# Performance work log

Hardware: AMD Instinct MI355X
Metric: run time of the kernel (lower is better)

## Reference

```python
import jax, jax.numpy as jnp
import numpy as np

B, N, FEAT, H, E, L = 4096, 64, 32, 128, 4, 3  # batch, node_num, node feat, hidden_dim, edge_dim, hidden_num


def setup_inputs() -> dict:
    key = jax.random.key(0)
    ks = jax.random.split(key, 12)
    s = 0.05
    x = jax.random.normal(ks[0], (B, N, FEAT), dtype=jnp.float32)
    adj = jax.random.uniform(ks[1], (B, E, N, N), dtype=jnp.float32)
    # per-node input/output embeddings (stacked over node index)
    in_w = jax.random.normal(ks[2], (N, FEAT, H), dtype=jnp.float32) * s
    in_b = jax.random.normal(ks[3], (N, H), dtype=jnp.float32) * s
    out_w = jax.random.normal(ks[4], (N, H, FEAT), dtype=jnp.float32) * s
    out_b = jax.random.normal(ks[5], (N, FEAT), dtype=jnp.float32) * s
    # relational GC weights per layer: (L, E, H, H) and bias (L, E, 1, H)
    gc_w = jax.random.normal(ks[6], (L, E, H, H), dtype=jnp.float32) * s
    gc_b = jax.random.normal(ks[7], (L, E, 1, H), dtype=jnp.float32) * s
    # GRU params, gate order [r, z, n] like torch
    w_ih = jax.random.normal(ks[8], (3 * H, H), dtype=jnp.float32) * s
    w_hh = jax.random.normal(ks[9], (3 * H, H), dtype=jnp.float32) * s
    b_ih = jax.random.normal(ks[10], (3 * H,), dtype=jnp.float32) * s
    b_hh = jax.random.normal(ks[11], (3 * H,), dtype=jnp.float32) * s
    return {"x": x, "adj": adj, "in_w": in_w, "in_b": in_b, "out_w": out_w,
            "out_b": out_b, "gc_w": gc_w, "gc_b": gc_b, "w_ih": w_ih,
            "w_hh": w_hh, "b_ih": b_ih, "b_hh": b_hh}


def _gru_step(xf, h, w_ih, w_hh, b_ih, b_hh):
    # xf, h: (B*N, H); single-timestep torch GRU cell
    gi = xf @ w_ih.T + b_ih
    gh = h @ w_hh.T + b_hh
    i_r, i_z, i_n = jnp.split(gi, 3, axis=-1)
    h_r, h_z, h_n = jnp.split(gh, 3, axis=-1)
    r = jax.nn.sigmoid(i_r + h_r)
    z = jax.nn.sigmoid(i_z + h_z)
    n = jnp.tanh(i_n + r * h_n)
    return (1.0 - z) * n + z * h


def reference(x, adj, in_w, in_b, out_w, out_b, gc_w, gc_b, w_ih, w_hh, b_ih, b_hh):
    # per-node input embedding: (B, N, FEAT) -> (B, N, H)
    h = jnp.einsum('bnd,ndh->bnh', x, in_w) + in_b
    hidden = h.reshape(-1, H)  # initial GRU hidden = embedded input
    cur = h
    for i in range(L):
        # relational GCN: per-edge-type projection + adjacency matmul + bias + relu + mean over edge types
        support = jnp.einsum('bid,edh->beih', cur, gc_w[i])
        out = jnp.einsum('beij,bejh->beih', adj, support) + gc_b[i]
        out = jax.nn.relu(out)
        agg = jnp.mean(out, axis=1)  # (B, N, H)
        hidden = _gru_step(agg.reshape(-1, H), hidden, w_ih, w_hh, b_ih, b_hh)
        cur = hidden.reshape(B, N, H)
    # per-node output embedding, zero-padded back to hidden width
    feats = jnp.einsum('bnh,nhd->bnd', cur, out_w) + out_b  # (B, N, FEAT)
    return jnp.pad(feats, ((0, 0), (0, 0), (0, H - FEAT)))
```

## Files before the change

### kernel.cpp

```cpp
#include <hip/hip_runtime.h>
#include <cstdint>

#define NBATCH 4096
#define NNODE  64
#define FEAT   32
#define H      128
#define NE     4
#define NL     3

typedef __attribute__((ext_vector_type(8))) short short8;
typedef __attribute__((ext_vector_type(4))) short short4v;
typedef __attribute__((ext_vector_type(4))) float f32x4;
typedef __attribute__((ext_vector_type(2))) float f32x2;
typedef unsigned long long u64;
typedef unsigned short ushort;

#define IMG_GC_ELEMS   (128 * 64)
#define IMG_GRU_ELEMS  (48 * 128)
#define IMG_GC_BYTES   (24 * IMG_GC_ELEMS * 2)
#define IMG_GRU_BYTES  (16 * IMG_GRU_ELEMS * 2)
#define WS_W_BYTES     (IMG_GC_BYTES + IMG_GRU_BYTES)
#define WIMG_SHORTS    (WS_W_BYTES / 2)
#define ADJ_IMG_ELEMS  4096
#define WS_FULL ((size_t)WS_W_BYTES + (size_t)NBATCH * NE * ADJ_IMG_ELEMS * 2)

__device__ __forceinline__ ushort f2b(float f) {
  union { float f; unsigned u; } v; v.f = f;
  unsigned u = v.u + 0x7FFFu + ((v.u >> 16) & 1u);
  return (ushort)(u >> 16);
}
__device__ __forceinline__ float b2f(ushort s) {
  union { unsigned u; float f; } v; v.u = ((unsigned)s) << 16;
  return v.f;
}
__device__ __forceinline__ unsigned cvtpk(float lo, float hi) {
  unsigned r;
  asm volatile("v_cvt_pk_bf16_f32 %0, %1, %2" : "=v"(r) : "v"(lo), "v"(hi));
  return r;
}
__device__ __forceinline__ u64 pk4(float a, float b, float c, float d) {
  return (u64)cvtpk(a, b) | ((u64)cvtpk(c, d) << 32);
}
__device__ __forceinline__ float sigm(float v) { return 1.0f / (1.0f + __expf(-v)); }
__device__ __forceinline__ float tanh_(float v) {
  v = fminf(fmaxf(v, -15.f), 15.f);
  float e = __expf(-2.f * v);
  return (1.f - e) / (1.f + e);
}
__device__ __forceinline__ int gidx128(int r, int g) { return r * 128 + ((g ^ (r & 7)) << 3); }
__device__ __forceinline__ int idx128(int r, int k) { return gidx128(r, k >> 3) + (k & 7); }
__device__ __forceinline__ int gidx64(int r, int g) { return r * 64 + (((g ^ (r & 7)) & 7) << 3); }

__device__ __forceinline__ short8 pack8f(const float* v) {
  union { unsigned u[4]; short8 s; } r;
  r.u[0] = cvtpk(v[0], v[1]); r.u[1] = cvtpk(v[2], v[3]);
  r.u[2] = cvtpk(v[4], v[5]); r.u[3] = cvtpk(v[6], v[7]);
  return r.s;
}

__device__ __forceinline__ void gll16(const void* g, void* l) {
  __builtin_amdgcn_global_load_lds(
      (const __attribute__((address_space(1))) unsigned int*)g,
      (__attribute__((address_space(3))) unsigned int*)l, 16, 0, 0);
}

#define STAGE(dst, src, NIT)                                             \
  do {                                                                   \
    _Pragma("unroll")                                                    \
    for (int it_ = 0; it_ < (NIT); ++it_) {                              \
      int off_ = (it_ * 4 + w) * 1024;                                   \
      gll16((const char*)(src) + off_ + lane * 16, (char*)(dst) + off_); \
    }                                                                    \
  } while (0)

#define BAR() do { asm volatile("s_waitcnt lgkmcnt(0)" ::: "memory"); \
                   __builtin_amdgcn_s_barrier(); } while (0)
#define VMW(N) do { asm volatile("s_waitcnt vmcnt(" #N ")" ::: "memory"); \
                    __builtin_amdgcn_sched_barrier(0); } while (0)
#define SB0() __builtin_amdgcn_sched_barrier(0)

__global__ __launch_bounds__(256, 2) void k_prep(
    const float* __restrict__ gc_w, const float* __restrict__ w_ih,
    const float* __restrict__ w_hh, ushort* __restrict__ ws)
{
  const int t = threadIdx.x;
  if (blockIdx.x < 24) {
    const int blk = blockIdx.x;
    const int kh = blk & 1, e = (blk >> 1) & 3, l = blk >> 3;
    const float* We = gc_w + (size_t)(l * NE + e) * H * H;
    ushort* dst = ws + (size_t)blk * IMG_GC_ELEMS;
    #pragma unroll
    for (int it = 0; it < 4; ++it) {
      int idx = t + it * 256;
      int r = idx >> 3, g = idx & 7;
      float v[8];
      #pragma unroll
      for (int j = 0; j < 8; ++j) v[j] = We[(kh * 64 + g * 8 + j) * H + r];
      *(short8*)&dst[gidx64(r, g)] = pack8f(v);
    }
  } else {
    const int blk = blockIdx.x - 24;
    const int c = blk & 7, m = blk >> 3;
    const float* Mat = m ? w_hh : w_ih;
    ushort* dst = ws + WIMG_SHORTS - IMG_GRU_BYTES / 2 + (size_t)blk * IMG_GRU_ELEMS;
    #pragma unroll
    for (int it = 0; it < 3; ++it) {
      int idx = t + it * 256;
      int rr = idx >> 4, g = idx & 15;
      int mrow = (rr >> 4) * H + 16 * c + (rr & 15);
      float v[8];
      #pragma unroll
      for (int j = 0; j < 8; ++j) v[j] = Mat[mrow * H + g * 8 + j];
      *(short8*)&dst[gidx128(rr, g)] = pack8f(v);
    }
  }
}

template <bool ADJIMG>
__global__ __launch_bounds__(256, 2) void k_inemb(
    const float* __restrict__ x, const float* __restrict__ in_w,
    const float* __restrict__ in_b, const float* __restrict__ adj,
    ushort* __restrict__ ws, float* __restrict__ out)
{
  __shared__ float s_wt[FEAT * H];
  __shared__ float s_x[64 * FEAT];
  const int t = threadIdx.x;
  const int n = blockIdx.x >> 6, bt = blockIdx.x & 63, b0 = bt * 64;
  const float* wsrc = in_w + (size_t)n * FEAT * H;
  #pragma unroll
  for (int it = 0; it < 4; ++it) {
    int i4 = t + it * 256;
    *(f32x4*)&s_wt[i4 * 4] = *(const f32x4*)&wsrc[i4 * 4];
  }
  {
    int r = t >> 2, q = t & 3;
    const float* xs = x + ((size_t)(b0 + r) * NNODE + n) * FEAT;
    *(f32x4*)&s_x[r * 32 + q * 8]     = *(const f32x4*)&xs[q * 8];
    *(f32x4*)&s_x[r * 32 + q * 8 + 4] = *(const f32x4*)&xs[q * 8 + 4];
  }
  __syncthreads();
  const int h2 = t & 63, rp = t >> 6;
  const float bi0 = in_b[n * H + 2 * h2], bi1 = in_b[n * H + 2 * h2 + 1];
  #pragma unroll 1
  for (int m = 0; m < 16; ++m) {
    int r = rp + 4 * m;
    float a0 = bi0, a1 = bi1;
    #pragma unroll
    for (int d = 0; d < 32; ++d) {
      float xv = s_x[r * 32 + d];
      f32x2 wv = *(const f32x2*)&s_wt[d * H + 2 * h2];
      a0 += xv * wv.x; a1 += xv * wv.y;
    }
    unsigned p = cvtpk(a0, a1);
    ushort* tail = (ushort*)(out + ((size_t)(b0 + r) * NNODE + n) * H + 64);
    *(unsigned*)(tail + 2 * h2) = p;
  }
  if (ADJIMG) {
    const float* ab = adj + (size_t)blockIdx.x * NE * NNODE * NNODE;
    ushort* dst = ws + WIMG_SHORTS + (size_t)blockIdx.x * NE * ADJ_IMG_ELEMS;
    #pragma unroll 1
    for (int q = 0; q < 8; ++q) {
      int gi = t + q * 256;
      int e = gi >> 9, idx = gi & 511, r = idx >> 3, g = idx & 7;
      const float* src = ab + e * 4096 + r * 64 + g * 8;
      float v[8];
      #pragma unroll
      for (int j = 0; j < 8; ++j) v[j] = src[j];
      *(short8*)&dst[e * ADJ_IMG_ELEMS + gidx64(r, g)] = pack8f(v);
    }
  }
}

template <bool ADJIMG>
__global__ __launch_bounds__(256, 2) void k_main(
    const float* __restrict__ adj,
    const float* __restrict__ gc_b,
    const float* __restrict__ b_ih, const float* __restrict__ b_hh,
    const ushort* __restrict__ wimg,
    float* __restrict__ out)
{
  __shared__ ushort s_u[128 * 64];
  __shared__ ushort s_stage[24576];
  __shared__ float s_bias[1280];

  ushort* w0    = s_stage;
  ushort* w1    = s_stage + 8192;
  ushort* sadj  = s_stage + 16384;
  ushort* gru0  = s_stage;
  ushort* gru1  = s_stage + 12288;

  const int t = threadIdx.x;
  const int b = blockIdx.x;
  const int w = t >> 6, lane = t & 63, lr = lane & 15, lq = lane >> 4;
  const int wm = w & 1, wn = w >> 1;
  float* outb = out + (size_t)b * NNODE * H;
  const ushort* img_gru = wimg + WIMG_SHORTS - IMG_GRU_BYTES / 2;
  const ushort* aimg = wimg + WIMG_SHORTS + (size_t)b * NE * ADJ_IMG_ELEMS;

  STAGE(w0, wimg, 4);
  short8 cur[2][4];
  #pragma unroll
  for (int rt = 0; rt < 2; ++rt)
    #pragma unroll
    for (int ks = 0; ks < 4; ++ks) {
      int node = 32 * wm + 16 * rt + lr;
      cur[rt][ks] = *(const short8*)((const ushort*)(outb + (size_t)node * H + 64) + 32 * ks + 8 * lq);
    }
  #pragma unroll
  for (int it = 0; it < 3; ++it) {
    int idx = t + it * 256;
    s_bias[512 + idx] = (idx < 384) ? b_ih[idx] : b_hh[idx - 384];
  }
  __syncthreads();

  #pragma unroll 1
  for (int layer = 0; layer < NL; ++layer) {
    f32x4 agg[2][4];
    #pragma unroll
    for (int mt = 0; mt < 2; ++mt)
      #pragma unroll
      for (int nt = 0; nt < 4; ++nt) agg[mt][nt] = f32x4{0.f, 0.f, 0.f, 0.f};

    #pragma unroll 1
    for (int e = 0; e < NE; ++e) {
      const ushort* img_e = wimg + (size_t)((layer * NE + e) * 2) * IMG_GC_ELEMS;

      if (e == 0) {
        s_bias[t]       = gc_b[layer * 512 + t];
        s_bias[t + 256] = gc_b[layer * 512 + t + 256];
      }
      STAGE(w1, img_e + IMG_GC_ELEMS, 4);
      SB0();
      if (ADJIMG) {
        STAGE(sadj, aimg + (size_t)e * ADJ_IMG_ELEMS, 2);
        SB0();
      } else {
        const float* adj_e = adj + (((size_t)b * NE + e) * NNODE * NNODE);
        #pragma unroll
        for (int it = 0; it < 2; ++it) {
          int idx = t + it * 256;
          int i = idx >> 3, g = idx & 7;
          const float* src = adj_e + i * 64 + g * 8;
          float v[8];
          #pragma unroll
          for (int j = 0; j < 8; ++j) v[j] = src[j];
          *(short8*)&sadj[gidx64(i, g)] = pack8f(v);
        }
      }
      f32x4 Sacc[2][4];
      #pragma unroll
      for (int mt = 0; mt < 2; ++mt)
        #pragma unroll
        for (int nt = 0; nt < 4; ++nt) Sacc[mt][nt] = f32x4{0.f, 0.f, 0.f, 0.f};
      if (ADJIMG) VMW(6);
      __builtin_amdgcn_s_setprio(1);
      #pragma unroll
      for (int ks = 0; ks < 2; ++ks) {
        #pragma unroll
        for (int nt = 0; nt < 4; ++nt) {
          short8 bb = *(const short8*)&w0[gidx64(64 * wn + 16 * nt + lr, ks * 4 + lq)];
          #pragma unroll
          for (int mt = 0; mt < 2; ++mt)
            Sacc[mt][nt] = __builtin_amdgcn_mfma_f32_16x16x32_bf16(cur[mt][ks], bb, Sacc[mt][nt], 0, 0, 0);
        }
      }
      __builtin_amdgcn_s_setprio(0);
      if (ADJIMG) { VMW(2); BAR(); } else __syncthreads();

      if (e < 3) { STAGE(w0, img_e + 2 * IMG_GC_ELEMS, 4); }
      else       { STAGE(gru0, img_gru, 3); }
      SB0();
      __builtin_amdgcn_s_setprio(1);
      #pragma unroll
      for (int ks = 0; ks < 2; ++ks) {
        #pragma unroll
        for (int nt = 0; nt < 4; ++nt) {
          short8 bb = *(const short8*)&w1[gidx64(64 * wn + 16 * nt + lr, ks * 4 + lq)];
          #pragma unroll
          for (int mt = 0; mt < 2; ++mt)
            Sacc[mt][nt] = __builtin_amdgcn_mfma_f32_16x16x32_bf16(cur[mt][2 + ks], bb, Sacc[mt][nt], 0, 0, 0);
        }
      }
      __builtin_amdgcn_s_setprio(0);
      #pragma unroll
      for (int mt = 0; mt < 2; ++mt) {
        int j0 = 32 * wm + 16 * mt + 4 * lq;
        #pragma unroll
        for (int nt = 0; nt < 4; ++nt) {
          int h = 64 * wn + 16 * nt + lr;
          *(u64*)&s_u[gidx64(h, j0 >> 3) + (j0 & 7)] =
              pk4(Sacc[mt][nt][0], Sacc[mt][nt][1], Sacc[mt][nt][2], Sacc[mt][nt][3]);
        }
      }
      if (ADJIMG) { if (e < 3) { VMW(4); } else { VMW(3); } BAR(); } else __syncthreads();

      if (e == 3) { STAGE(gru0 + 6144, img_gru + IMG_GRU_ELEMS, 3); SB0(); }
      {
        f32x4 Oacc[2][4];
        #pragma unroll
        for (int mt = 0; mt < 2; ++mt)
          #pragma unroll
          for (int nt = 0; nt < 4; ++nt) Oacc[mt][nt] = f32x4{0.f, 0.f, 0.f, 0.f};
        __builtin_amdgcn_s_setprio(1);
        #pragma unroll
        for (int ks = 0; ks < 2; ++ks) {
          short8 a[2];
          #pragma unroll
          for (int mt = 0; mt < 2; ++mt)
            a[mt] = *(const short8*)&sadj[gidx64(32 * wm + 16 * mt + lr, ks * 4 + lq)];
          #pragma unroll
          for (int nt = 0; nt < 4; ++nt) {
            short8 bb = *(const short8*)&s_u[gidx64(64 * wn + 16 * nt + lr, ks * 4 + lq)];
            #pragma unroll
            for (int mt = 0; mt < 2; ++mt)
              Oacc[mt][nt] = __builtin_amdgcn_mfma_f32_16x16x32_bf16(a[mt], bb, Oacc[mt][nt], 0, 0, 0);
          }
        }
        __builtin_amdgcn_s_setprio(0);
        #pragma unroll
        for (int mt = 0; mt < 2; ++mt)
          #pragma unroll
          for (int nt = 0; nt < 4; ++nt) {
            float bias = s_bias[e * 128 + 64 * wn + 16 * nt + lr];
            #pragma unroll
            for (int r = 0; r < 4; ++r)
              agg[mt][nt][r] += 0.25f * fmaxf(Oacc[mt][nt][r] + bias, 0.f);
          }
      }
      if (ADJIMG) { BAR(); } else __syncthreads();
    }

    #pragma unroll
    for (int mt = 0; mt < 2; ++mt)
      #pragma unroll
      for (int nt = 0; nt < 4; ++nt) {
        int h = 64 * wn + 16 * nt + lr;
        #pragma unroll
        for (int r = 0; r < 4; ++r)
          s_u[idx128(32 * wm + 16 * mt + 4 * lq + r, h)] = f2b(agg[mt][nt][r]);
      }
    __syncthreads();

    #pragma unroll 1
    for (int p = 0; p < 4; ++p) {
      const int cc = 2 * p + wn;
      const ushort* ihb = gru0 + wn * 6144;
      const ushort* hhb = gru1 + wn * 6144;
      STAGE(gru1, img_gru + (size_t)(8 + 2 * p) * IMG_GRU_ELEMS, 3);
      STAGE(gru1 + 6144, img_gru + (size_t)(8 + 2 * p + 1) * IMG_GRU_ELEMS, 3);
      SB0();
      short4v holdv[2];
      #pragma unroll
      for (int nst = 0; nst < 2; ++nst) {
        int node = 16 * (2 * wm + nst) + lr;
        holdv[nst] = *(const short4v*)((const ushort*)(outb + (size_t)node * H + 64) + 16 * cc + 4 * lq);
      }
      f32x4 gi[3][2];
      #pragma unroll
      for (int tg = 0; tg < 3; ++tg)
        #pragma unroll
        for (int nst = 0; nst < 2; ++nst) gi[tg][nst] = f32x4{0.f, 0.f, 0.f, 0.f};
      __builtin_amdgcn_s_setprio(1);
      #pragma unroll
      for (int ks = 0; ks < 4; ++ks) {
        short8 bb[2];
        #pragma unroll
        for (int nst = 0; nst < 2; ++nst)
          bb[nst] = *(const short8*)&s_u[gidx128(16 * (2 * wm + nst) + lr, ks * 4 + lq)];
        #pragma unroll
        for (int tg = 0; tg < 3; ++tg) {
          short8 a = *(const short8*)&ihb[gidx128(16 * tg + lr, ks * 4 + lq)];
          #pragma unroll
          for (int nst = 0; nst < 2; ++nst)
            gi[tg][nst] = __builtin_amdgcn_mfma_f32_16x16x32_bf16(a, bb[nst], gi[tg][nst], 0, 0, 0);
        }
      }
      __builtin_amdgcn_s_setprio(0);
      __syncthreads();

      if (p < 3) {
        STAGE(gru0, img_gru + (size_t)(2 * (p + 1)) * IMG_GRU_ELEMS, 3);
        STAGE(gru0 + 6144, img_gru + (size_t)(2 * (p + 1) + 1) * IMG_GRU_ELEMS, 3);
      } else if (layer < 2) {
        STAGE(w0, wimg + (size_t)((layer + 1) * NE * 2) * IMG_GC_ELEMS, 4);
      }
      SB0();
      f32x4 gh[3][2];
      #pragma unroll
      for (int tg = 0; tg < 3; ++tg)
        #pragma unroll
        for (int nst = 0; nst < 2; ++nst) gh[tg][nst] = f32x4{0.f, 0.f, 0.f, 0.f};
      __builtin_amdgcn_s_setprio(1);
      #pragma unroll
      for (int ks = 0; ks < 4; ++ks) {
        #pragma unroll
        for (int tg = 0; tg < 3; ++tg) {
          short8 a = *(const short8*)&hhb[gidx128(16 * tg + lr, ks * 4 + lq)];
          #pragma unroll
          for (int nst = 0; nst < 2; ++nst)
            gh[tg][nst] = __builtin_amdgcn_mfma_f32_16x16x32_bf16(a, cur[nst][ks], gh[tg][nst], 0, 0, 0);
        }
      }
      __builtin_amdgcn_s_setprio(0);
      #pragma unroll
      for (int nst = 0; nst < 2; ++nst) {
        int node = 16 * (2 * wm + nst) + lr;
        float hf[4];
        #pragma unroll
        for (int r = 0; r < 4; ++r) {
          int mH = 16 * cc + 4 * lq + r;
          float rg = sigm(gi[0][nst][r] + s_bias[512 + mH] + gh[0][nst][r] + s_bias[896 + mH]);
          float zg = sigm(gi[1][nst][r] + s_bias[640 + mH] + gh[1][nst][r] + s_bias[1024 + mH]);
          float ng = tanh_(gi[2][nst][r] + s_bias[768 + mH] + rg * (gh[2][nst][r] + s_bias[1152 + mH]));
          float hold = b2f((ushort)holdv[nst][r]);
          hf[r] = (1.f - zg) * ng + zg * hold;
        }
        *(u64*)((ushort*)(outb + (size_t)node * H + 64) + 16 * cc + 4 * lq) =
            pk4(hf[0], hf[1], hf[2], hf[3]);
      }
      __syncthreads();
    }

    if (layer < 2) {
      #pragma unroll
      for (int rt = 0; rt < 2; ++rt)
        #pragma unroll
        for (int ks = 0; ks < 4; ++ks) {
          int node = 32 * wm + 16 * rt + lr;
          cur[rt][ks] = *(const short8*)((const ushort*)(outb + (size_t)node * H + 64) + 32 * ks + 8 * lq);
        }
    }
  }
}

__global__ __launch_bounds__(256, 2) void k_outemb(
    const float* __restrict__ out_w, const float* __restrict__ out_b,
    float* __restrict__ out)
{
  __shared__ float s_wt[H * FEAT];
  __shared__ float s_c[64 * 132];
  const int t = threadIdx.x;
  const int n = blockIdx.x >> 6, bt = blockIdx.x & 63, b0 = bt * 64;
  const float* wsrc = out_w + (size_t)n * H * FEAT;
  #pragma unroll
  for (int it = 0; it < 4; ++it) {
    int i4 = t + it * 256;
    *(f32x4*)&s_wt[i4 * 4] = *(const f32x4*)&wsrc[i4 * 4];
  }
  #pragma unroll
  for (int it = 0; it < 4; ++it) {
    int idx = t + it * 256;
    int r = idx >> 4, g = idx & 15;
    const ushort* tail = (const ushort*)(out + ((size_t)(b0 + r) * NNODE + n) * H + 64);
    short8 v = *(const short8*)(tail + g * 8);
    #pragma unroll
    for (int j = 0; j < 8; ++j) s_c[r * 132 + g * 8 + j] = b2f((ushort)v[j]);
  }
  __syncthreads();
  const int d = t & 31, rq = t >> 5;
  const float bias = out_b[n * FEAT + d];
  float accs[8];
  #pragma unroll
  for (int m = 0; m < 8; ++m) {
    int r = rq + 8 * m;
    float a = bias;
    #pragma unroll 8
    for (int k = 0; k < H; ++k) a += s_c[r * 132 + k] * s_wt[k * FEAT + d];
    accs[m] = a;
  }
  #pragma unroll
  for (int m = 0; m < 8; ++m) {
    int r = rq + 8 * m;
    out[((size_t)(b0 + r) * NNODE + n) * H + d] = accs[m];
  }
  #pragma unroll
  for (int q = 0; q < 6; ++q) {
    int idx = t + q * 256;
    int r = idx / 24, c4 = idx - r * 24;
    *(f32x4*)&out[((size_t)(b0 + r) * NNODE + n) * H + FEAT + c4 * 4] =
        f32x4{0.f, 0.f, 0.f, 0.f};
  }
}

extern "C" void kernel_launch(void* const* d_in, const int* in_sizes, int n_in,
                              void* d_out, int out_size, void* d_ws, size_t ws_size,
                              hipStream_t stream) {
  const float* x     = (const float*)d_in[0];
  const float* adj   = (const float*)d_in[1];
  const float* in_w  = (const float*)d_in[2];
  const float* in_b  = (const float*)d_in[3];
  const float* out_w = (const float*)d_in[4];
  const float* out_b = (const float*)d_in[5];
  const float* gc_w  = (const float*)d_in[6];
  const float* gc_b  = (const float*)d_in[7];
  const float* w_ih  = (const float*)d_in[8];
  const float* w_hh  = (const float*)d_in[9];
  const float* b_ih  = (const float*)d_in[10];
  const float* b_hh  = (const float*)d_in[11];
  (void)in_sizes; (void)n_in; (void)out_size;
  ushort* wimg = (ushort*)d_ws;
  const bool full = ws_size >= WS_FULL;
  hipLaunchKernelGGL(k_prep, dim3(40), dim3(256), 0, stream, gc_w, w_ih, w_hh, wimg);
  if (full) {
    hipLaunchKernelGGL(k_inemb<true>, dim3(NBATCH), dim3(256), 0, stream,
                       x, in_w, in_b, adj, wimg, (float*)d_out);
    hipLaunchKernelGGL(k_main<true>, dim3(NBATCH), dim3(256), 0, stream,
                       adj, gc_b, b_ih, b_hh, wimg, (float*)d_out);
  } else {
    hipLaunchKernelGGL(k_inemb<false>, dim3(NBATCH), dim3(256), 0, stream,
                       x, in_w, in_b, adj, wimg, (float*)d_out);
    hipLaunchKernelGGL(k_main<false>, dim3(NBATCH), dim3(256), 0, stream,
                       adj, gc_b, b_ih, b_hh, wimg, (float*)d_out);
  }
  hipLaunchKernelGGL(k_outemb, dim3(NBATCH), dim3(256), 0, stream, out_w, out_b, (float*)d_out);
}
```

Measured before the change: 763.9 us.

## Run main GNN kernel with 8 waves and triple-buffered weight staging

Doubles the main kernel's block to 512 threads so each wave owns a smaller output tile (half the columns in GCN, one node group in GRU). It reorganises LDS into three rotating weight buffers plus a separate adjacency buffer, so the next edge-type's weight halves can be prefetched earlier. GC biases move into registers and GRU bias indexing is compacted. The aim is more latency hiding and occupancy, at the cost of more waves contending for barriers and higher LDS use per block, which may limit how many blocks fit per CU.

```diff
diff --git a/kernel.cpp b/kernel.cpp
--- a/kernel.cpp
+++ b/kernel.cpp
@@ -64,11 +64,11 @@
       (__attribute__((address_space(3))) unsigned int*)l, 16, 0, 0);
 }
 
-#define STAGE(dst, src, NIT)                                             \
+#define STAGE8(dst, src, NIT)                                            \
   do {                                                                   \
     _Pragma("unroll")                                                    \
     for (int it_ = 0; it_ < (NIT); ++it_) {                              \
-      int off_ = (it_ * 4 + w) * 1024;                                   \
+      int off_ = (it_ * 8 + w) * 1024;                                   \
       gll16((const char*)(src) + off_ + lane * 16, (char*)(dst) + off_); \
     }                                                                    \
   } while (0)
@@ -78,6 +78,8 @@
 #define VMW(N) do { asm volatile("s_waitcnt vmcnt(" #N ")" ::: "memory"); \
                     __builtin_amdgcn_sched_barrier(0); } while (0)
 #define SB0() __builtin_amdgcn_sched_barrier(0)
+
+#define MFMA16(A, B, C) __builtin_amdgcn_mfma_f32_16x16x32_bf16((A), (B), (C), 0, 0, 0)
 
 __global__ __launch_bounds__(256, 2) void k_prep(
     const float* __restrict__ gc_w, const float* __restrict__ w_ih,
@@ -172,113 +174,111 @@
 }
 
 template <bool ADJIMG>
-__global__ __launch_bounds__(256, 2) void k_main(
+__global__ __launch_bounds__(512, 4) void k_main(
     const float* __restrict__ adj,
     const float* __restrict__ gc_b,
     const float* __restrict__ b_ih, const float* __restrict__ b_hh,
     const ushort* __restrict__ wimg,
     float* __restrict__ out)
 {
-  __shared__ ushort s_u[128 * 64];
-  __shared__ ushort s_stage[24576];
-  __shared__ float s_bias[1280];
-
-  ushort* w0    = s_stage;
-  ushort* w1    = s_stage + 8192;
-  ushort* sadj  = s_stage + 16384;
-  ushort* gru0  = s_stage;
-  ushort* gru1  = s_stage + 12288;
+  __shared__ ushort s_stage[28672];
+  __shared__ ushort s_u[8192];
+  __shared__ float  s_bias[768];
+
+  ushort* const R0   = s_stage;
+  ushort* const R1   = s_stage + 8192;
+  ushort* const R2   = s_stage + 16384;
+  ushort* const adjb = s_stage + 24576;
+  ushort* const G0   = s_stage;
+  ushort* const G1   = s_stage + 12288;
 
   const int t = threadIdx.x;
   const int b = blockIdx.x;
   const int w = t >> 6, lane = t & 63, lr = lane & 15, lq = lane >> 4;
-  const int wm = w & 1, wn = w >> 1;
+  const int wm = w & 1, wq = w >> 1;
+  const int cpar = wq & 1, nsub = wq >> 1;
+  const int ng = 2 * wm + nsub;
   float* outb = out + (size_t)b * NNODE * H;
-  const ushort* img_gru = wimg + WIMG_SHORTS - IMG_GRU_BYTES / 2;
+  const ushort* img_gruih = wimg + 196608;
+  const ushort* img_gruhh = wimg + 196608 + 8 * IMG_GRU_ELEMS;
   const ushort* aimg = wimg + WIMG_SHORTS + (size_t)b * NE * ADJ_IMG_ELEMS;
 
-  STAGE(w0, wimg, 4);
-  short8 cur[2][4];
-  #pragma unroll
-  for (int rt = 0; rt < 2; ++rt)
-    #pragma unroll
-    for (int ks = 0; ks < 4; ++ks) {
-      int node = 32 * wm + 16 * rt + lr;
-      cur[rt][ks] = *(const short8*)((const ushort*)(outb + (size_t)node * H + 64) + 32 * ks + 8 * lq);
-    }
-  #pragma unroll
-  for (int it = 0; it < 3; ++it) {
-    int idx = t + it * 256;
-    s_bias[512 + idx] = (idx < 384) ? b_ih[idx] : b_hh[idx - 384];
-  }
+  ushort* const K0s[4] = {R0, R2, R1, R0};
+  ushort* const K1s[4] = {R1, R0, R2, R1};
+
+  STAGE8(R0, wimg, 2);
+  STAGE8(R1, wimg + 8192, 2);
+  short8 curA[4], curB[4], curS[4];
+  #pragma unroll
+  for (int ks = 0; ks < 4; ++ks) {
+    curA[ks] = *(const short8*)((const ushort*)(outb + (size_t)(32 * wm + lr) * H + 64) + 32 * ks + 8 * lq);
+    curB[ks] = *(const short8*)((const ushort*)(outb + (size_t)(32 * wm + 16 + lr) * H + 64) + 32 * ks + 8 * lq);
+    curS[ks] = *(const short8*)((const ushort*)(outb + (size_t)(16 * ng + lr) * H + 64) + 32 * ks + 8 * lq);
+  }
+  float gb[4][2];
+  #pragma unroll
+  for (int e = 0; e < 4; ++e) {
+    gb[e][0] = gc_b[e * 128 + 32 * wq + lr];
+    gb[e][1] = gc_b[e * 128 + 32 * wq + 16 + lr];
+  }
+  s_bias[t] = (t < 384) ? b_ih[t] : b_hh[t - 384];
+  if (t < 256) s_bias[512 + t] = b_hh[t + 128];
   __syncthreads();
 
   #pragma unroll 1
   for (int layer = 0; layer < NL; ++layer) {
-    f32x4 agg[2][4];
-    #pragma unroll
-    for (int mt = 0; mt < 2; ++mt)
-      #pragma unroll
-      for (int nt = 0; nt < 4; ++nt) agg[mt][nt] = f32x4{0.f, 0.f, 0.f, 0.f};
-
-    #pragma unroll 1
-    for (int e = 0; e < NE; ++e) {
-      const ushort* img_e = wimg + (size_t)((layer * NE + e) * 2) * IMG_GC_ELEMS;
-
-      if (e == 0) {
-        s_bias[t]       = gc_b[layer * 512 + t];
-        s_bias[t + 256] = gc_b[layer * 512 + t + 256];
-      }
-      STAGE(w1, img_e + IMG_GC_ELEMS, 4);
-      SB0();
+    f32x4 agg[2][2];
+    #pragma unroll
+    for (int mt = 0; mt < 2; ++mt) {
+      #pragma unroll
+      for (int nt = 0; nt < 2; ++nt) agg[mt][nt] = f32x4{0.f, 0.f, 0.f, 0.f};
+    }
+
+    #pragma unroll
+    for (int e = 0; e < 4; ++e) {
       if (ADJIMG) {
-        STAGE(sadj, aimg + (size_t)e * ADJ_IMG_ELEMS, 2);
+        STAGE8(adjb, aimg + (size_t)e * ADJ_IMG_ELEMS, 1);
         SB0();
       } else {
         const float* adj_e = adj + (((size_t)b * NE + e) * NNODE * NNODE);
-        #pragma unroll
-        for (int it = 0; it < 2; ++it) {
-          int idx = t + it * 256;
-          int i = idx >> 3, g = idx & 7;
-          const float* src = adj_e + i * 64 + g * 8;
-          float v[8];
-          #pragma unroll
-          for (int j = 0; j < 8; ++j) v[j] = src[j];
-          *(short8*)&sadj[gidx64(i, g)] = pack8f(v);
-        }
-      }
-      f32x4 Sacc[2][4];
-      #pragma unroll
-      for (int mt = 0; mt < 2; ++mt)
-        #pragma unroll
-        for (int nt = 0; nt < 4; ++nt) Sacc[mt][nt] = f32x4{0.f, 0.f, 0.f, 0.f};
-      if (ADJIMG) VMW(6);
+        int i = t >> 3, g = t & 7;
+        const float* src = adj_e + i * 64 + g * 8;
+        float v[8];
+        #pragma unroll
+        for (int j = 0; j < 8; ++j) v[j] = src[j];
+        *(short8*)&adjb[gidx64(i, g)] = pack8f(v);
+      }
+      f32x4 Sacc[2][2];
+      #pragma unroll
+      for (int mt = 0; mt < 2; ++mt) {
+        #pragma unroll
+        for (int nt = 0; nt < 2; ++nt) Sacc[mt][nt] = f32x4{0.f, 0.f, 0.f, 0.f};
+      }
       __builtin_amdgcn_s_setprio(1);
       #pragma unroll
       for (int ks = 0; ks < 2; ++ks) {
         #pragma unroll
-        for (int nt = 0; nt < 4; ++nt) {
-          short8 bb = *(const short8*)&w0[gidx64(64 * wn + 16 * nt + lr, ks * 4 + lq)];
-          #pragma unroll
-          for (int mt = 0; mt < 2; ++mt)
-            Sacc[mt][nt] = __builtin_amdgcn_mfma_f32_16x16x32_bf16(cur[mt][ks], bb, Sacc[mt][nt], 0, 0, 0);
+        for (int nt = 0; nt < 2; ++nt) {
+          short8 bb = *(const short8*)&K0s[e][gidx64(32 * wq + 16 * nt + lr, ks * 4 + lq)];
+          Sacc[0][nt] = MFMA16(curA[ks], bb, Sacc[0][nt]);
+          Sacc[1][nt] = MFMA16(curB[ks], bb, Sacc[1][nt]);
         }
       }
       __builtin_amdgcn_s_setprio(0);
-      if (ADJIMG) { VMW(2); BAR(); } else __syncthreads();
-
-      if (e < 3) { STAGE(w0, img_e + 2 * IMG_GC_ELEMS, 4); }
-      else       { STAGE(gru0, img_gru, 3); }
-      SB0();
+      if (ADJIMG) { VMW(1); BAR(); } else __syncthreads();
+
+      if (e < 3) {
+        STAGE8(K0s[e + 1], wimg + (size_t)((layer * 4 + e + 1) * 2) * IMG_GC_ELEMS, 2);
+        SB0();
+      }
       __builtin_amdgcn_s_setprio(1);
       #pragma unroll
       for (int ks = 0; ks < 2; ++ks) {
         #pragma unroll
-        for (int nt = 0; nt < 4; ++nt) {
-          short8 bb = *(const short8*)&w1[gidx64(64 * wn + 16 * nt + lr, ks * 4 + lq)];
-          #pragma unroll
-          for (int mt = 0; mt < 2; ++mt)
-            Sacc[mt][nt] = __builtin_amdgcn_mfma_f32_16x16x32_bf16(cur[mt][2 + ks], bb, Sacc[mt][nt], 0, 0, 0);
+        for (int nt = 0; nt < 2; ++nt) {
+          short8 bb = *(const short8*)&K1s[e][gidx64(32 * wq + 16 * nt + lr, ks * 4 + lq)];
+          Sacc[0][nt] = MFMA16(curA[2 + ks], bb, Sacc[0][nt]);
+          Sacc[1][nt] = MFMA16(curB[2 + ks], bb, Sacc[1][nt]);
         }
       }
       __builtin_amdgcn_s_setprio(0);
@@ -286,149 +286,137 @@
       for (int mt = 0; mt < 2; ++mt) {
         int j0 = 32 * wm + 16 * mt + 4 * lq;
         #pragma unroll
-        for (int nt = 0; nt < 4; ++nt) {
-          int h = 64 * wn + 16 * nt + lr;
+        for (int nt = 0; nt < 2; ++nt) {
+          int h = 32 * wq + 16 * nt + lr;
           *(u64*)&s_u[gidx64(h, j0 >> 3) + (j0 & 7)] =
               pk4(Sacc[mt][nt][0], Sacc[mt][nt][1], Sacc[mt][nt][2], Sacc[mt][nt][3]);
         }
       }
-      if (ADJIMG) { if (e < 3) { VMW(4); } else { VMW(3); } BAR(); } else __syncthreads();
-
-      if (e == 3) { STAGE(gru0 + 6144, img_gru + IMG_GRU_ELEMS, 3); SB0(); }
+      if (ADJIMG) { if (e < 3) { VMW(2); } else { VMW(0); } BAR(); } else __syncthreads();
+
+      if (e < 3) {
+        STAGE8(K1s[e + 1], wimg + (size_t)((layer * 4 + e + 1) * 2 + 1) * IMG_GC_ELEMS, 2);
+        SB0();
+      } else {
+        STAGE8(G0, img_gruih, 3);
+        STAGE8(G1, img_gruhh, 3);
+        SB0();
+      }
       {
-        f32x4 Oacc[2][4];
-        #pragma unroll
-        for (int mt = 0; mt < 2; ++mt)
+        f32x4 Oacc[2][2];
+        #pragma unroll
+        for (int mt = 0; mt < 2; ++mt) {
           #pragma unroll
-          for (int nt = 0; nt < 4; ++nt) Oacc[mt][nt] = f32x4{0.f, 0.f, 0.f, 0.f};
+          for (int nt = 0; nt < 2; ++nt) Oacc[mt][nt] = f32x4{0.f, 0.f, 0.f, 0.f};
+        }
         __builtin_amdgcn_s_setprio(1);
         #pragma unroll
         for (int ks = 0; ks < 2; ++ks) {
-          short8 a[2];
+          short8 a0 = *(const short8*)&adjb[gidx64(32 * wm + lr, ks * 4 + lq)];
+          short8 a1 = *(const short8*)&adjb[gidx64(32 * wm + 16 + lr, ks * 4 + lq)];
           #pragma unroll
-          for (int mt = 0; mt < 2; ++mt)
-            a[mt] = *(const short8*)&sadj[gidx64(32 * wm + 16 * mt + lr, ks * 4 + lq)];
+          for (int nt = 0; nt < 2; ++nt) {
+            short8 bb = *(const short8*)&s_u[gidx64(32 * wq + 16 * nt + lr, ks * 4 + lq)];
+            Oacc[0][nt] = MFMA16(a0, bb, Oacc[0][nt]);
+            Oacc[1][nt] = MFMA16(a1, bb, Oacc[1][nt]);
+          }
+        }
+        __builtin_amdgcn_s_setprio(0);
+        #pragma unroll
+        for (int mt = 0; mt < 2; ++mt) {
           #pragma unroll
-          for (int nt = 0; nt < 4; ++nt) {
-            short8 bb = *(const short8*)&s_u[gidx64(64 * wn + 16 * nt + lr, ks * 4 + lq)];
-            #pragma unroll
-            for (int mt = 0; mt < 2; ++mt)
-              Oacc[mt][nt] = __builtin_amdgcn_mfma_f32_16x16x32_bf16(a[mt], bb, Oacc[mt][nt], 0, 0, 0);
-          }
-        }
-        __builtin_amdgcn_s_setprio(0);
-        #pragma unroll
-        for (int mt = 0; mt < 2; ++mt)
-          #pragma unroll
-          for (int nt = 0; nt < 4; ++nt) {
-            float bias = s_bias[e * 128 + 64 * wn + 16 * nt + lr];
+          for (int nt = 0; nt < 2; ++nt) {
             #pragma unroll
             for (int r = 0; r < 4; ++r)
-              agg[mt][nt][r] += 0.25f * fmaxf(Oacc[mt][nt][r] + bias, 0.f);
+              agg[mt][nt][r] += 0.25f * fmaxf(Oacc[mt][nt][r] + gb[e][nt], 0.f);
           }
-      }
-      if (ADJIMG) { BAR(); } else __syncthreads();
-    }
-
-    #pragma unroll
-    for (int mt = 0; mt < 2; ++mt)
-      #pragma unroll
-      for (int nt = 0; nt < 4; ++nt) {
-        int h = 64 * wn + 16 * nt + lr;
+        }
+      }
+      if (ADJIMG) { if (e < 3) { VMW(2); } BAR(); } else __syncthreads();
+    }
+
+    #pragma unroll
+    for (int mt = 0; mt < 2; ++mt) {
+      #pragma unroll
+      for (int nt = 0; nt < 2; ++nt) {
+        int h = 32 * wq + 16 * nt + lr;
         #pragma unroll
         for (int r = 0; r < 4; ++r)
           s_u[idx128(32 * wm + 16 * mt + 4 * lq + r, h)] = f2b(agg[mt][nt][r]);
       }
+    }
     __syncthreads();
 
     #pragma unroll 1
     for (int p = 0; p < 4; ++p) {
-      const int cc = 2 * p + wn;
-      const ushort* ihb = gru0 + wn * 6144;
-      const ushort* hhb = gru1 + wn * 6144;
-      STAGE(gru1, img_gru + (size_t)(8 + 2 * p) * IMG_GRU_ELEMS, 3);
-      STAGE(gru1 + 6144, img_gru + (size_t)(8 + 2 * p + 1) * IMG_GRU_ELEMS, 3);
+      const int cc = 2 * p + cpar;
+      if (p >= 1) { STAGE8(G1, img_gruhh + (size_t)p * 12288, 3); }
       SB0();
-      short4v holdv[2];
-      #pragma unroll
-      for (int nst = 0; nst < 2; ++nst) {
-        int node = 16 * (2 * wm + nst) + lr;
-        holdv[nst] = *(const short4v*)((const ushort*)(outb + (size_t)node * H + 64) + 16 * cc + 4 * lq);
-      }
-      f32x4 gi[3][2];
-      #pragma unroll
-      for (int tg = 0; tg < 3; ++tg)
-        #pragma unroll
-        for (int nst = 0; nst < 2; ++nst) gi[tg][nst] = f32x4{0.f, 0.f, 0.f, 0.f};
+      short4v holdv = *(const short4v*)((const ushort*)(outb + (size_t)(16 * ng + lr) * H + 64) + 16 * cc + 4 * lq);
+      f32x4 gi[3], gh[3];
+      #pragma unroll
+      for (int tg = 0; tg < 3; ++tg) gi[tg] = f32x4{0.f, 0.f, 0.f, 0.f};
+      const ushort* ihb = G0 + cpar * 6144;
       __builtin_amdgcn_s_setprio(1);
       #pragma unroll
       for (int ks = 0; ks < 4; ++ks) {
-        short8 bb[2];
-        #pragma unroll
-        for (int nst = 0; nst < 2; ++nst)
-          bb[nst] = *(const short8*)&s_u[gidx128(16 * (2 * wm + nst) + lr, ks * 4 + lq)];
+        short8 bb = *(const short8*)&s_u[gidx128(16 * ng + lr, ks * 4 + lq)];
         #pragma unroll
         for (int tg = 0; tg < 3; ++tg) {
           short8 a = *(const short8*)&ihb[gidx128(16 * tg + lr, ks * 4 + lq)];
-          #pragma unroll
-          for (int nst = 0; nst < 2; ++nst)
-            gi[tg][nst] = __builtin_amdgcn_mfma_f32_16x16x32_bf16(a, bb[nst], gi[tg][nst], 0, 0, 0);
+          gi[tg] = MFMA16(a, bb, gi[tg]);
         }
       }
       __builtin_amdgcn_s_setprio(0);
       __syncthreads();
 
-      if (p < 3) {
-        STAGE(gru0, img_gru + (size_t)(2 * (p + 1)) * IMG_GRU_ELEMS, 3);
-        STAGE(gru0 + 6144, img_gru + (size_t)(2 * (p + 1) + 1) * IMG_GRU_ELEMS, 3);
-      } else if (layer < 2) {
-        STAGE(w0, wimg + (size_t)((layer + 1) * NE * 2) * IMG_GC_ELEMS, 4);
-      }
+      if (p < 3)          { STAGE8(G0, img_gruih + (size_t)(p + 1) * 12288, 3); }
+      else if (layer < 2) { STAGE8(R0, wimg + (size_t)((layer + 1) * 8) * IMG_GC_ELEMS, 2); }
       SB0();
-      f32x4 gh[3][2];
-      #pragma unroll
-      for (int tg = 0; tg < 3; ++tg)
-        #pragma unroll
-        for (int nst = 0; nst < 2; ++nst) gh[tg][nst] = f32x4{0.f, 0.f, 0.f, 0.f};
+      #pragma unroll
+      for (int tg = 0; tg < 3; ++tg) gh[tg] = f32x4{0.f, 0.f, 0.f, 0.f};
+      const ushort* hhb = G1 + cpar * 6144;
       __builtin_amdgcn_s_setprio(1);
       #pragma unroll
       for (int ks = 0; ks < 4; ++ks) {
         #pragma unroll
         for (int tg = 0; tg < 3; ++tg) {
           short8 a = *(const short8*)&hhb[gidx128(16 * tg + lr, ks * 4 + lq)];
-          #pragma unroll
-          for (int nst = 0; nst < 2; ++nst)
-            gh[tg][nst] = __builtin_amdgcn_mfma_f32_16x16x32_bf16(a, cur[nst][ks], gh[tg][nst], 0, 0, 0);
+          gh[tg] = MFMA16(a, curS[ks], gh[tg]);
         }
       }
       __builtin_amdgcn_s_setprio(0);
-      #pragma unroll
-      for (int nst = 0; nst < 2; ++nst) {
-        int node = 16 * (2 * wm + nst) + lr;
+      {
         float hf[4];
         #pragma unroll
         for (int r = 0; r < 4; ++r) {
           int mH = 16 * cc + 4 * lq + r;
-          float rg = sigm(gi[0][nst][r] + s_bias[512 + mH] + gh[0][nst][r] + s_bias[896 + mH]);
-          float zg = sigm(gi[1][nst][r] + s_bias[640 + mH] + gh[1][nst][r] + s_bias[1024 + mH]);
-          float ng = tanh_(gi[2][nst][r] + s_bias[768 + mH] + rg * (gh[2][nst][r] + s_bias[1152 + mH]));
-          float hold = b2f((ushort)holdv[nst][r]);
-          hf[r] = (1.f - zg) * ng + zg * hold;
-        }
-        *(u64*)((ushort*)(outb + (size_t)node * H + 64) + 16 * cc + 4 * lq) =
+          float rg = sigm(gi[0][r] + s_bias[mH] + gh[0][r] + s_bias[384 + mH]);
+          float zg = sigm(gi[1][r] + s_bias[128 + mH] + gh[1][r] + s_bias[512 + mH]);
+          float nn = tanh_(gi[2][r] + s_bias[256 + mH] + rg * (gh[2][r] + s_bias[640 + mH]));
+          hf[r] = (1.f - zg) * nn + zg * b2f((ushort)holdv[r]);
+        }
+        *(u64*)((ushort*)(outb + (size_t)(16 * ng + lr) * H + 64) + 16 * cc + 4 * lq) =
             pk4(hf[0], hf[1], hf[2], hf[3]);
       }
       __syncthreads();
     }
 
     if (layer < 2) {
-      #pragma unroll
-      for (int rt = 0; rt < 2; ++rt)
-        #pragma unroll
-        for (int ks = 0; ks < 4; ++ks) {
-          int node = 32 * wm + 16 * rt + lr;
-          cur[rt][ks] = *(const short8*)((const ushort*)(outb + (size_t)node * H + 64) + 32 * ks + 8 * lq);
-        }
+      STAGE8(R1, wimg + (size_t)((layer + 1) * 8 + 1) * IMG_GC_ELEMS, 2);
+      SB0();
+      #pragma unroll
+      for (int ks = 0; ks < 4; ++ks) {
+        curA[ks] = *(const short8*)((const ushort*)(outb + (size_t)(32 * wm + lr) * H + 64) + 32 * ks + 8 * lq);
+        curB[ks] = *(const short8*)((const ushort*)(outb + (size_t)(32 * wm + 16 + lr) * H + 64) + 32 * ks + 8 * lq);
+        curS[ks] = *(const short8*)((const ushort*)(outb + (size_t)(16 * ng + lr) * H + 64) + 32 * ks + 8 * lq);
+      }
+      #pragma unroll
+      for (int e = 0; e < 4; ++e) {
+        gb[e][0] = gc_b[(layer + 1) * 512 + e * 128 + 32 * wq + lr];
+        gb[e][1] = gc_b[(layer + 1) * 512 + e * 128 + 32 * wq + 16 + lr];
+      }
+      __syncthreads();
     }
   }
 }
@@ -504,12 +492,12 @@
   if (full) {
     hipLaunchKernelGGL(k_inemb<true>, dim3(NBATCH), dim3(256), 0, stream,
                        x, in_w, in_b, adj, wimg, (float*)d_out);
-    hipLaunchKernelGGL(k_main<true>, dim3(NBATCH), dim3(256), 0, stream,
+    hipLaunchKernelGGL(k_main<true>, dim3(NBATCH), dim3(512), 0, stream,
                        adj, gc_b, b_ih, b_hh, wimg, (float*)d_out);
   } else {
     hipLaunchKernelGGL(k_inemb<false>, dim3(NBATCH), dim3(256), 0, stream,
                        x, in_w, in_b, adj, wimg, (float*)d_out);
-    hipLaunchKernelGGL(k_main<false>, dim3(NBATCH), dim3(256), 0, stream,
+    hipLaunchKernelGGL(k_main<false>, dim3(NBATCH), dim3(512), 0, stream,
                        adj, gc_b, b_ih, b_hh, wimg, (float*)d_out);
   }
   hipLaunchKernelGGL(k_outemb, dim3(NBATCH), dim3(256), 0, stream, out_w, out_b, (float*)d_out);
```

New measurement: 1.254 ms. 64.2% more time.

## Switch GCN matmuls to 32x32x16 MFMA and restructure weight staging schedule

Applied to the files above, without the earlier changes.

Replaces the 16x16x32 bf16 MFMA tiles in the relational GCN support and adjacency products with 32x32x16 tiles, changing per-wave fragment layouts, LDS read patterns and the bias/relu accumulation mapping. Weight-image staging is rescheduled so both W0 and W1 halves are prefetched earlier (at kernel start and at end of the previous layer), and the per-edge loop is fully unrolled. The aim is fewer MFMA issues and LDS fragment loads per FLOP and better overlap of global-to-LDS copies with compute. The cost is more accumulator registers (f32x16) and subtler vmcnt/barrier sequencing, which could hurt occupancy or correctness.

```diff
diff --git a/kernel.cpp b/kernel.cpp
--- a/kernel.cpp
+++ b/kernel.cpp
@@ -10,6 +10,7 @@
 
 typedef __attribute__((ext_vector_type(8))) short short8;
 typedef __attribute__((ext_vector_type(4))) short short4v;
+typedef __attribute__((ext_vector_type(16))) float f32x16;
 typedef __attribute__((ext_vector_type(4))) float f32x4;
 typedef __attribute__((ext_vector_type(2))) float f32x2;
 typedef unsigned long long u64;
@@ -48,8 +49,13 @@
   return (1.f - e) / (1.f + e);
 }
 __device__ __forceinline__ int gidx128(int r, int g) { return r * 128 + ((g ^ (r & 7)) << 3); }
-__device__ __forceinline__ int idx128(int r, int k) { return gidx128(r, k >> 3) + (k & 7); }
 __device__ __forceinline__ int gidx64(int r, int g) { return r * 64 + (((g ^ (r & 7)) & 7) << 3); }
+__device__ __forceinline__ f32x16 z16() {
+  f32x16 z;
+  #pragma unroll
+  for (int i = 0; i < 16; ++i) z[i] = 0.f;
+  return z;
+}
 
 __device__ __forceinline__ short8 pack8f(const float* v) {
   union { unsigned u[4]; short8 s; } r;
@@ -78,6 +84,9 @@
 #define VMW(N) do { asm volatile("s_waitcnt vmcnt(" #N ")" ::: "memory"); \
                     __builtin_amdgcn_sched_barrier(0); } while (0)
 #define SB0() __builtin_amdgcn_sched_barrier(0)
+
+#define MFMA16(A, B, C) __builtin_amdgcn_mfma_f32_16x16x32_bf16((A), (B), (C), 0, 0, 0)
+#define MFMA32(A, B, C) __builtin_amdgcn_mfma_f32_32x32x16_bf16((A), (B), (C), 0, 0, 0)
 
 __global__ __launch_bounds__(256, 2) void k_prep(
     const float* __restrict__ gc_w, const float* __restrict__ w_ih,
@@ -179,33 +188,30 @@
     const ushort* __restrict__ wimg,
     float* __restrict__ out)
 {
-  __shared__ ushort s_u[128 * 64];
   __shared__ ushort s_stage[24576];
-  __shared__ float s_bias[1280];
-
-  ushort* w0    = s_stage;
-  ushort* w1    = s_stage + 8192;
-  ushort* sadj  = s_stage + 16384;
-  ushort* gru0  = s_stage;
-  ushort* gru1  = s_stage + 12288;
-
-  const int t = threadIdx.x;
-  const int b = blockIdx.x;
-  const int w = t >> 6, lane = t & 63, lr = lane & 15, lq = lane >> 4;
+  __shared__ ushort s_u[8192];
+  __shared__ float  s_bias[1280];
+
+  ushort* const W0   = s_stage;
+  ushort* const W1   = s_stage + 8192;
+  ushort* const adjb = s_stage + 16384;
+  ushort* const G0   = s_stage;
+  ushort* const G1   = s_stage + 12288;
+
+  const int t = threadIdx.x, b = blockIdx.x;
+  const int w = t >> 6, lane = t & 63, l31 = lane & 31, hi = lane >> 5;
+  const int lr = lane & 15, lq = lane >> 4;
   const int wm = w & 1, wn = w >> 1;
   float* outb = out + (size_t)b * NNODE * H;
   const ushort* img_gru = wimg + WIMG_SHORTS - IMG_GRU_BYTES / 2;
   const ushort* aimg = wimg + WIMG_SHORTS + (size_t)b * NE * ADJ_IMG_ELEMS;
 
-  STAGE(w0, wimg, 4);
-  short8 cur[2][4];
-  #pragma unroll
-  for (int rt = 0; rt < 2; ++rt)
-    #pragma unroll
-    for (int ks = 0; ks < 4; ++ks) {
-      int node = 32 * wm + 16 * rt + lr;
-      cur[rt][ks] = *(const short8*)((const ushort*)(outb + (size_t)node * H + 64) + 32 * ks + 8 * lq);
-    }
+  STAGE(W0, wimg, 4);
+  STAGE(W1, wimg + IMG_GC_ELEMS, 4);
+  short8 cur32[8];
+  #pragma unroll
+  for (int ks = 0; ks < 8; ++ks)
+    cur32[ks] = *(const short8*)((const ushort*)(outb + (size_t)(32 * wm + l31) * H + 64) + 16 * ks + 8 * hi);
   #pragma unroll
   for (int it = 0; it < 3; ++it) {
     int idx = t + it * 256;
@@ -215,24 +221,19 @@
 
   #pragma unroll 1
   for (int layer = 0; layer < NL; ++layer) {
-    f32x4 agg[2][4];
-    #pragma unroll
-    for (int mt = 0; mt < 2; ++mt)
-      #pragma unroll
-      for (int nt = 0; nt < 4; ++nt) agg[mt][nt] = f32x4{0.f, 0.f, 0.f, 0.f};
-
-    #pragma unroll 1
-    for (int e = 0; e < NE; ++e) {
+    f32x16 agg[2];
+    agg[0] = z16(); agg[1] = z16();
+
+    #pragma unroll
+    for (int e = 0; e < 4; ++e) {
       const ushort* img_e = wimg + (size_t)((layer * NE + e) * 2) * IMG_GC_ELEMS;
 
       if (e == 0) {
         s_bias[t]       = gc_b[layer * 512 + t];
         s_bias[t + 256] = gc_b[layer * 512 + t + 256];
       }
-      STAGE(w1, img_e + IMG_GC_ELEMS, 4);
-      SB0();
       if (ADJIMG) {
-        STAGE(sadj, aimg + (size_t)e * ADJ_IMG_ELEMS, 2);
+        STAGE(adjb, aimg + (size_t)e * ADJ_IMG_ELEMS, 2);
         SB0();
       } else {
         const float* adj_e = adj + (((size_t)b * NE + e) * NNODE * NNODE);
@@ -244,122 +245,111 @@
           float v[8];
           #pragma unroll
           for (int j = 0; j < 8; ++j) v[j] = src[j];
-          *(short8*)&sadj[gidx64(i, g)] = pack8f(v);
-        }
-      }
-      f32x4 Sacc[2][4];
-      #pragma unroll
-      for (int mt = 0; mt < 2; ++mt)
-        #pragma unroll
-        for (int nt = 0; nt < 4; ++nt) Sacc[mt][nt] = f32x4{0.f, 0.f, 0.f, 0.f};
-      if (ADJIMG) VMW(6);
+          *(short8*)&adjb[gidx64(i, g)] = pack8f(v);
+        }
+      }
+      f32x16 Sacc[2];
+      Sacc[0] = z16(); Sacc[1] = z16();
       __builtin_amdgcn_s_setprio(1);
       #pragma unroll
-      for (int ks = 0; ks < 2; ++ks) {
-        #pragma unroll
-        for (int nt = 0; nt < 4; ++nt) {
-          short8 bb = *(const short8*)&w0[gidx64(64 * wn + 16 * nt + lr, ks * 4 + lq)];
-          #pragma unroll
-          for (int mt = 0; mt < 2; ++mt)
-            Sacc[mt][nt] = __builtin_amdgcn_mfma_f32_16x16x32_bf16(cur[mt][ks], bb, Sacc[mt][nt], 0, 0, 0);
+      for (int ks = 0; ks < 4; ++ks) {
+        #pragma unroll
+        for (int q = 0; q < 2; ++q) {
+          short8 bb = *(const short8*)&W0[gidx64(32 * (2 * wn + q) + l31, 2 * ks + hi)];
+          Sacc[q] = MFMA32(cur32[ks], bb, Sacc[q]);
         }
       }
       __builtin_amdgcn_s_setprio(0);
       if (ADJIMG) { VMW(2); BAR(); } else __syncthreads();
 
-      if (e < 3) { STAGE(w0, img_e + 2 * IMG_GC_ELEMS, 4); }
-      else       { STAGE(gru0, img_gru, 3); }
-      SB0();
+      if (e < 3) { STAGE(W0, img_e + 2 * IMG_GC_ELEMS, 4); SB0(); }
+      else       { STAGE(G0, img_gru, 3); SB0(); }
       __builtin_amdgcn_s_setprio(1);
       #pragma unroll
-      for (int ks = 0; ks < 2; ++ks) {
-        #pragma unroll
-        for (int nt = 0; nt < 4; ++nt) {
-          short8 bb = *(const short8*)&w1[gidx64(64 * wn + 16 * nt + lr, ks * 4 + lq)];
+      for (int ks = 0; ks < 4; ++ks) {
+        #pragma unroll
+        for (int q = 0; q < 2; ++q) {
+          short8 bb = *(const short8*)&W1[gidx64(32 * (2 * wn + q) + l31, 2 * ks + hi)];
+          Sacc[q] = MFMA32(cur32[4 + ks], bb, Sacc[q]);
+        }
+      }
+      __builtin_amdgcn_s_setprio(0);
+      #pragma unroll
+      for (int q = 0; q < 2; ++q) {
+        int h = 32 * (2 * wn + q) + l31;
+        #pragma unroll
+        for (int u = 0; u < 4; ++u) {
+          *(u64*)&s_u[gidx64(h, 4 * wm + u) + 4 * hi] =
+              pk4(Sacc[q][4 * u], Sacc[q][4 * u + 1], Sacc[q][4 * u + 2], Sacc[q][4 * u + 3]);
+        }
+      }
+      if (ADJIMG) { if (e < 3) { VMW(4); } else { VMW(3); } BAR(); } else __syncthreads();
+
+      if (e < 3) { STAGE(W1, img_e + 3 * IMG_GC_ELEMS, 4); SB0(); }
+      else       { STAGE(G0 + 6144, img_gru + IMG_GRU_ELEMS, 3); SB0(); }
+      {
+        f32x16 Oacc[2];
+        Oacc[0] = z16(); Oacc[1] = z16();
+        __builtin_amdgcn_s_setprio(1);
+        #pragma unroll
+        for (int ks = 0; ks < 4; ++ks) {
+          short8 badj = *(const short8*)&adjb[gidx64(32 * wm + l31, 2 * ks + hi)];
           #pragma unroll
-          for (int mt = 0; mt < 2; ++mt)
-            Sacc[mt][nt] = __builtin_amdgcn_mfma_f32_16x16x32_bf16(cur[mt][2 + ks], bb, Sacc[mt][nt], 0, 0, 0);
-        }
-      }
-      __builtin_amdgcn_s_setprio(0);
-      #pragma unroll
-      for (int mt = 0; mt < 2; ++mt) {
-        int j0 = 32 * wm + 16 * mt + 4 * lq;
-        #pragma unroll
-        for (int nt = 0; nt < 4; ++nt) {
-          int h = 64 * wn + 16 * nt + lr;
-          *(u64*)&s_u[gidx64(h, j0 >> 3) + (j0 & 7)] =
-              pk4(Sacc[mt][nt][0], Sacc[mt][nt][1], Sacc[mt][nt][2], Sacc[mt][nt][3]);
+          for (int q = 0; q < 2; ++q) {
+            short8 aS = *(const short8*)&s_u[gidx64(32 * (2 * wn + q) + l31, 2 * ks + hi)];
+            Oacc[q] = MFMA32(aS, badj, Oacc[q]);
+          }
+        }
+        __builtin_amdgcn_s_setprio(0);
+        #pragma unroll
+        for (int q = 0; q < 2; ++q) {
+          #pragma unroll
+          for (int u = 0; u < 4; ++u) {
+            f32x4 b4 = *(const f32x4*)&s_bias[e * 128 + 32 * (2 * wn + q) + 8 * u + 4 * hi];
+            #pragma unroll
+            for (int v = 0; v < 4; ++v)
+              agg[q][4 * u + v] += 0.25f * fmaxf(Oacc[q][4 * u + v] + b4[v], 0.f);
+          }
         }
       }
       if (ADJIMG) { if (e < 3) { VMW(4); } else { VMW(3); } BAR(); } else __syncthreads();
-
-      if (e == 3) { STAGE(gru0 + 6144, img_gru + IMG_GRU_ELEMS, 3); SB0(); }
-      {
-        f32x4 Oacc[2][4];
-        #pragma unroll
-        for (int mt = 0; mt < 2; ++mt)
-          #pragma unroll
-          for (int nt = 0; nt < 4; ++nt) Oacc[mt][nt] = f32x4{0.f, 0.f, 0.f, 0.f};
-        __builtin_amdgcn_s_setprio(1);
-        #pragma unroll
-        for (int ks = 0; ks < 2; ++ks) {
-          short8 a[2];
-          #pragma unroll
-          for (int mt = 0; mt < 2; ++mt)
-            a[mt] = *(const short8*)&sadj[gidx64(32 * wm + 16 * mt + lr, ks * 4 + lq)];
-          #pragma unroll
-          for (int nt = 0; nt < 4; ++nt) {
-            short8 bb = *(const short8*)&s_u[gidx64(64 * wn + 16 * nt + lr, ks * 4 + lq)];
-            #pragma unroll
-            for (int mt = 0; mt < 2; ++mt)
-              Oacc[mt][nt] = __builtin_amdgcn_mfma_f32_16x16x32_bf16(a[mt], bb, Oacc[mt][nt], 0, 0, 0);
-          }
-        }
-        __builtin_amdgcn_s_setprio(0);
-        #pragma unroll
-        for (int mt = 0; mt < 2; ++mt)
-          #pragma unroll
-          for (int nt = 0; nt < 4; ++nt) {
-            float bias = s_bias[e * 128 + 64 * wn + 16 * nt + lr];
-            #pragma unroll
-            for (int r = 0; r < 4; ++r)
-              agg[mt][nt][r] += 0.25f * fmaxf(Oacc[mt][nt][r] + bias, 0.f);
-          }
-      }
-      if (ADJIMG) { BAR(); } else __syncthreads();
-    }
-
-    #pragma unroll
-    for (int mt = 0; mt < 2; ++mt)
-      #pragma unroll
-      for (int nt = 0; nt < 4; ++nt) {
-        int h = 64 * wn + 16 * nt + lr;
-        #pragma unroll
-        for (int r = 0; r < 4; ++r)
-          s_u[idx128(32 * wm + 16 * mt + 4 * lq + r, h)] = f2b(agg[mt][nt][r]);
-      }
+    }
+
+    #pragma unroll
+    for (int q = 0; q < 2; ++q) {
+      #pragma unroll
+      for (int u = 0; u < 4; ++u) {
+        *(u64*)&s_u[gidx128(32 * wm + l31, 4 * (2 * wn + q) + u) + 4 * hi] =
+            pk4(agg[q][4 * u], agg[q][4 * u + 1], agg[q][4 * u + 2], agg[q][4 * u + 3]);
+      }
+    }
+    short8 c16[2][4];
+    #pragma unroll
+    for (int nst = 0; nst < 2; ++nst) {
+      #pragma unroll
+      for (int ks = 0; ks < 4; ++ks)
+        c16[nst][ks] = *(const short8*)((const ushort*)(outb + (size_t)(16 * (2 * wm + nst) + lr) * H + 64) + 32 * ks + 8 * lq);
+    }
     __syncthreads();
 
     #pragma unroll 1
     for (int p = 0; p < 4; ++p) {
       const int cc = 2 * p + wn;
-      const ushort* ihb = gru0 + wn * 6144;
-      const ushort* hhb = gru1 + wn * 6144;
-      STAGE(gru1, img_gru + (size_t)(8 + 2 * p) * IMG_GRU_ELEMS, 3);
-      STAGE(gru1 + 6144, img_gru + (size_t)(8 + 2 * p + 1) * IMG_GRU_ELEMS, 3);
+      STAGE(G1, img_gru + (size_t)(8 + 2 * p) * IMG_GRU_ELEMS, 3);
+      STAGE(G1 + 6144, img_gru + (size_t)(8 + 2 * p + 1) * IMG_GRU_ELEMS, 3);
       SB0();
+      if (ADJIMG) { VMW(6); }
       short4v holdv[2];
       #pragma unroll
-      for (int nst = 0; nst < 2; ++nst) {
-        int node = 16 * (2 * wm + nst) + lr;
-        holdv[nst] = *(const short4v*)((const ushort*)(outb + (size_t)node * H + 64) + 16 * cc + 4 * lq);
-      }
-      f32x4 gi[3][2];
-      #pragma unroll
-      for (int tg = 0; tg < 3; ++tg)
+      for (int nst = 0; nst < 2; ++nst)
+        holdv[nst] = *(const short4v*)((const ushort*)(outb + (size_t)(16 * (2 * wm + nst) + lr) * H + 64) + 16 * cc + 4 * lq);
+      f32x4 gi[3][2], gh[3][2];
+      #pragma unroll
+      for (int tg = 0; tg < 3; ++tg) {
         #pragma unroll
         for (int nst = 0; nst < 2; ++nst) gi[tg][nst] = f32x4{0.f, 0.f, 0.f, 0.f};
+      }
+      const ushort* ihb = G0 + wn * 6144;
       __builtin_amdgcn_s_setprio(1);
       #pragma unroll
       for (int ks = 0; ks < 4; ++ks) {
@@ -372,24 +362,25 @@
           short8 a = *(const short8*)&ihb[gidx128(16 * tg + lr, ks * 4 + lq)];
           #pragma unroll
           for (int nst = 0; nst < 2; ++nst)
-            gi[tg][nst] = __builtin_amdgcn_mfma_f32_16x16x32_bf16(a, bb[nst], gi[tg][nst], 0, 0, 0);
+            gi[tg][nst] = MFMA16(a, bb[nst], gi[tg][nst]);
         }
       }
       __builtin_amdgcn_s_setprio(0);
       __syncthreads();
 
       if (p < 3) {
-        STAGE(gru0, img_gru + (size_t)(2 * (p + 1)) * IMG_GRU_ELEMS, 3);
-        STAGE(gru0 + 6144, img_gru + (size_t)(2 * (p + 1) + 1) * IMG_GRU_ELEMS, 3);
+        STAGE(G0, img_gru + (size_t)(2 * (p + 1)) * IMG_GRU_ELEMS, 3);
+        STAGE(G0 + 6144, img_gru + (size_t)(2 * (p + 1) + 1) * IMG_GRU_ELEMS, 3);
       } else if (layer < 2) {
-        STAGE(w0, wimg + (size_t)((layer + 1) * NE * 2) * IMG_GC_ELEMS, 4);
+        STAGE(W0, wimg + (size_t)((layer + 1) * NE * 2) * IMG_GC_ELEMS, 4);
       }
       SB0();
-      f32x4 gh[3][2];
-      #pragma unroll
-      for (int tg = 0; tg < 3; ++tg)
+      #pragma unroll
+      for (int tg = 0; tg < 3; ++tg) {
         #pragma unroll
         for (int nst = 0; nst < 2; ++nst) gh[tg][nst] = f32x4{0.f, 0.f, 0.f, 0.f};
+      }
+      const ushort* hhb = G1 + wn * 6144;
       __builtin_amdgcn_s_setprio(1);
       #pragma unroll
       for (int ks = 0; ks < 4; ++ks) {
@@ -398,7 +389,7 @@
           short8 a = *(const short8*)&hhb[gidx128(16 * tg + lr, ks * 4 + lq)];
           #pragma unroll
           for (int nst = 0; nst < 2; ++nst)
-            gh[tg][nst] = __builtin_amdgcn_mfma_f32_16x16x32_bf16(a, cur[nst][ks], gh[tg][nst], 0, 0, 0);
+            gh[tg][nst] = MFMA16(a, c16[nst][ks], gh[tg][nst]);
         }
       }
       __builtin_amdgcn_s_setprio(0);
@@ -412,8 +403,7 @@
           float rg = sigm(gi[0][nst][r] + s_bias[512 + mH] + gh[0][nst][r] + s_bias[896 + mH]);
           float zg = sigm(gi[1][nst][r] + s_bias[640 + mH] + gh[1][nst][r] + s_bias[1024 + mH]);
           float ng = tanh_(gi[2][nst][r] + s_bias[768 + mH] + rg * (gh[2][nst][r] + s_bias[1152 + mH]));
-          float hold = b2f((ushort)holdv[nst][r]);
-          hf[r] = (1.f - zg) * ng + zg * hold;
+          hf[r] = (1.f - zg) * ng + zg * b2f((ushort)holdv[nst][r]);
         }
         *(u64*)((ushort*)(outb + (size_t)node * H + 64) + 16 * cc + 4 * lq) =
             pk4(hf[0], hf[1], hf[2], hf[3]);
@@ -422,13 +412,12 @@
     }
 
     if (layer < 2) {
-      #pragma unroll
-      for (int rt = 0; rt < 2; ++rt)
-        #pragma unroll
-        for (int ks = 0; ks < 4; ++ks) {
-          int node = 32 * wm + 16 * rt + lr;
-          cur[rt][ks] = *(const short8*)((const ushort*)(outb + (size_t)node * H + 64) + 32 * ks + 8 * lq);
-        }
+      STAGE(W1, wimg + (size_t)((layer + 1) * NE * 2 + 1) * IMG_GC_ELEMS, 4);
+      SB0();
+      #pragma unroll
+      for (int ks = 0; ks < 8; ++ks)
+        cur32[ks] = *(const short8*)((const ushort*)(outb + (size_t)(32 * wm + l31) * H + 64) + 16 * ks + 8 * hi);
+      __syncthreads();
     }
   }
 }
```

New measurement: 808.8 us. +5.9%, slower.
